# Optimization experiments

Measured on AMD Instinct MI355X. Metric: run time of the kernel, lower is better.

The kernel has to match this reference:

```python
import jax, jax.numpy as jnp
import numpy as np

N_HEAD = 16
N_KV = 4
ROT = 128  # rotary_dim == head_dim
BASE = 10000
N_CTX = 1024


def make_sincos(n_ctx, rotary_dim, base):
    # GPT-NeoX style (rotary_adjacent_pairs=False): freq repeated twice
    pos = jnp.arange(n_ctx, dtype=jnp.float32)
    dim = jnp.arange(rotary_dim // 2, dtype=jnp.float32)
    freq = jnp.float32(base) ** (dim / (rotary_dim / 2))
    freq = jnp.tile(freq, 2)  # [rotary_dim]
    angles = pos[:, None] / freq[None, :]  # [n_ctx, rotary_dim]
    return jnp.sin(angles), jnp.cos(angles)


def setup_inputs() -> dict:
    key = jax.random.key(0)
    ks = jax.random.split(key, 5)
    B, T, C = 8, 1024, 2048
    r = N_HEAD // N_KV
    Ckv = C // r
    s = 0.02
    x = jax.random.normal(ks[0], (B, T, C), jnp.float32)
    wq = jax.random.normal(ks[1], (C, C), jnp.float32) * s
    wk = jax.random.normal(ks[2], (C, Ckv), jnp.float32) * s
    wv = jax.random.normal(ks[3], (C, Ckv), jnp.float32) * s
    wo = jax.random.normal(ks[4], (C, C), jnp.float32) * s
    sin, cos = make_sincos(N_CTX, ROT, BASE)
    return dict(x=x, wq=wq, wk=wk, wv=wv, wo=wo, sin=sin, cos=cos)


def _rope(x, sin, cos):
    # x: [B, H, T, hd]; rotary applied to first ROT dims (here ROT == hd)
    T = x.shape[2]
    n = ROT // 2
    x_rot = x[..., :ROT]
    x_pass = x[..., ROT:]
    # rotate_every_two (NeoX style): [x0..x_{n-1}, x_n..] -> [-x_n.., x0..]
    x_flip = jnp.concatenate([-x_rot[..., n:], x_rot[..., :n]], axis=-1)
    c = cos[None, None, :T, :]
    s = sin[None, None, :T, :]
    x_rotated = x_rot * c + x_flip * s
    return jnp.concatenate([x_rotated, x_pass], axis=-1)


def reference(x, wq, wk, wv, wo, sin, cos):
    B, T, C = x.shape
    H = N_HEAD
    hd = C // H
    r = H // N_KV
    q = (x @ wq).reshape(B, T, H, hd).transpose(0, 2, 1, 3)  # [B,H,T,hd]
    # Original: repeat_interleave along seq dim then view(B,T,H,hd).
    # Equivalent to tiling the kv channel vector r times per position.
    k = jnp.tile(x @ wk, (1, 1, r)).reshape(B, T, H, hd).transpose(0, 2, 1, 3)
    v = jnp.tile(x @ wv, (1, 1, r)).reshape(B, T, H, hd).transpose(0, 2, 1, 3)
    q = _rope(q, sin, cos)
    k = _rope(k, sin, cos)
    att = jnp.einsum('bhqd,bhkd->bhqk', q, k) / jnp.sqrt(jnp.float32(hd))
    causal = jnp.tril(jnp.ones((T, T), dtype=bool))
    att = jnp.where(causal[None, None], att, -jnp.inf)
    att = jax.nn.softmax(att, axis=-1)
    y = jnp.einsum('bhqk,bhkd->bhqd', att, v)
    y = y.transpose(0, 2, 1, 3).reshape(B, T, C)
    return y @ wo
```

## Files before the change

kernel.cpp:

```cpp
#include <hip/hip_runtime.h>

typedef __attribute__((ext_vector_type(8))) short short8;
typedef __attribute__((ext_vector_type(4))) float f32x4;

#define B_    8
#define T_    1024
#define C_    2048
#define H_    16
#define HKV_  4
#define HD_   128
#define M_    8192
#define NQKV_ 3072
#define KDIM_ 2048

__device__ __forceinline__ unsigned short f2bf(float f) {
  unsigned u = __float_as_uint(f);
  u += 0x7FFF + ((u >> 16) & 1);
  return (unsigned short)(u >> 16);
}
__device__ __forceinline__ float bf2f(unsigned short h) {
  return __uint_as_float(((unsigned)h) << 16);
}

__device__ __forceinline__ void async16(const unsigned short* g, unsigned short* l) {
  __builtin_amdgcn_global_load_lds(
      (const unsigned int __attribute__((address_space(1)))*)g,
      (unsigned int __attribute__((address_space(3)))*)l,
      16, 0, 0);
}

__global__ __launch_bounds__(256) void cvt_bf16_kernel(const float* __restrict__ in,
                                                       unsigned short* __restrict__ out) {
  int idx = blockIdx.x * 256 + threadIdx.x;
  float4 v = ((const float4*)in)[idx];
  ushort4 o;
  o.x = f2bf(v.x); o.y = f2bf(v.y); o.z = f2bf(v.z); o.w = f2bf(v.w);
  ((ushort4*)out)[idx] = o;
}

__global__ __launch_bounds__(256) void tpose_f32_bf16(const float* __restrict__ in,
                                                      unsigned short* __restrict__ out,
                                                      int Cc, int ldo) {
  __shared__ unsigned short tile[32][33];
  int c0 = blockIdx.x * 32, r0 = blockIdx.y * 32;
  int tx = threadIdx.x, ty = threadIdx.y;
#pragma unroll
  for (int j = 0; j < 4; j++)
    tile[ty + j * 8][tx] = f2bf(in[(size_t)(r0 + ty + j * 8) * Cc + c0 + tx]);
  __syncthreads();
#pragma unroll
  for (int j = 0; j < 4; j++)
    out[(size_t)(c0 + ty + j * 8) * ldo + r0 + tx] = tile[tx][ty + j * 8];
}

__global__ __launch_bounds__(256) void vtpose(const unsigned short* __restrict__ qkv,
                                              unsigned short* __restrict__ vt) {
  __shared__ unsigned short tile[32][33];
  int b = blockIdx.z;
  int c0 = blockIdx.x * 32, t0 = blockIdx.y * 32;
  int tx = threadIdx.x, ty = threadIdx.y;
  const unsigned short* src = qkv + (size_t)b * T_ * NQKV_ + 2560;
#pragma unroll
  for (int j = 0; j < 4; j++)
    tile[ty + j * 8][tx] = src[(size_t)(t0 + ty + j * 8) * NQKV_ + c0 + tx];
  __syncthreads();
  unsigned short* dst = vt + (size_t)b * 512 * T_;
#pragma unroll
  for (int j = 0; j < 4; j++)
    dst[(size_t)(c0 + ty + j * 8) * T_ + t0 + tx] = tile[tx][ty + j * 8];
}

__global__ __launch_bounds__(256) void rope_kernel(const unsigned short* __restrict__ qkv,
                                                   const float* __restrict__ sinp,
                                                   const float* __restrict__ cosp,
                                                   unsigned short* __restrict__ qatt,
                                                   unsigned short* __restrict__ katt) {
  int m = blockIdx.x;
  int b = m >> 10, t = m & 1023;
  int tid = threadIdx.x;
  int d = tid & 63;
  const unsigned short* row = qkv + (size_t)m * NQKV_;
  float c0 = cosp[t * 128 + d], s0 = sinp[t * 128 + d];
  float c1 = cosp[t * 128 + d + 64], s1 = sinp[t * 128 + d + 64];
#pragma unroll
  for (int h0 = 0; h0 < 16; h0 += 4) {
    int h = h0 + (tid >> 6);
    float x0 = bf2f(row[h * 128 + d]);
    float x1 = bf2f(row[h * 128 + d + 64]);
    size_t o = ((size_t)(b * 16 + h) * 1024 + t) * 128 + d;
    qatt[o]      = f2bf(x0 * c0 - x1 * s0);
    qatt[o + 64] = f2bf(x1 * c1 + x0 * s1);
  }
  {
    int kh = tid >> 6;
    float x0 = bf2f(row[2048 + kh * 128 + d]);
    float x1 = bf2f(row[2048 + kh * 128 + d + 64]);
    size_t o = ((size_t)(b * 4 + kh) * 1024 + t) * 128 + d;
    katt[o]      = f2bf(x0 * c0 - x1 * s0);
    katt[o + 64] = f2bf(x1 * c1 + x0 * s1);
  }
}

template <int OUTF32>
__global__ __launch_bounds__(256) void gemm_bf16(const unsigned short* __restrict__ A,
                                                 const unsigned short* __restrict__ BT,
                                                 void* __restrict__ Cout, int N) {
  __shared__ unsigned short lA[128 * 32];
  __shared__ unsigned short lB[128 * 32];
  const int K = KDIM_;
  int tid = threadIdx.x;
  int lane = tid & 63;
  int w = tid >> 6;
  int quad = lane >> 4, l16 = lane & 15;
  int bm = blockIdx.y, bn = blockIdx.x;
  const unsigned short* Ab = A + (size_t)bm * 128 * K;
  const unsigned short* Bb = BT + (size_t)bn * 128 * K;
  int i0 = tid, i1 = tid + 256;
  int ra0 = i0 >> 2, ca0 = (i0 & 3) * 8;
  int ra1 = i1 >> 2, ca1 = (i1 & 3) * 8;
  int wm = (w >> 1) * 64, wn = (w & 1) * 64;
  f32x4 acc[4][4] = {};
  for (int k0 = 0; k0 < K; k0 += 32) {
    __syncthreads();
    async16(Ab + (size_t)ra0 * K + k0 + ca0, &lA[i0 * 8]);
    async16(Ab + (size_t)ra1 * K + k0 + ca1, &lA[i1 * 8]);
    async16(Bb + (size_t)ra0 * K + k0 + ca0, &lB[i0 * 8]);
    async16(Bb + (size_t)ra1 * K + k0 + ca1, &lB[i1 * 8]);
    __syncthreads();
    short8 af[4], bfr[4];
#pragma unroll
    for (int mt = 0; mt < 4; mt++)
      af[mt] = *(const short8*)&lA[(wm + mt * 16 + l16) * 32 + quad * 8];
#pragma unroll
    for (int nt = 0; nt < 4; nt++)
      bfr[nt] = *(const short8*)&lB[(wn + nt * 16 + l16) * 32 + quad * 8];
#pragma unroll
    for (int mt = 0; mt < 4; mt++)
#pragma unroll
      for (int nt = 0; nt < 4; nt++)
        acc[mt][nt] = __builtin_amdgcn_mfma_f32_16x16x32_bf16(af[mt], bfr[nt], acc[mt][nt], 0, 0, 0);
  }
#pragma unroll
  for (int mt = 0; mt < 4; mt++) {
#pragma unroll
    for (int nt = 0; nt < 4; nt++) {
      int n = bn * 128 + wn + nt * 16 + l16;
#pragma unroll
      for (int r = 0; r < 4; r++) {
        int m = bm * 128 + wm + mt * 16 + quad * 4 + r;
        if (OUTF32)
          ((float*)Cout)[(size_t)m * N + n] = acc[mt][nt][r];
        else
          ((unsigned short*)Cout)[(size_t)m * N + n] = f2bf(acc[mt][nt][r]);
      }
    }
  }
}

__global__ __launch_bounds__(256, 2) void attn_kernel(const unsigned short* __restrict__ Q,
                                                      const unsigned short* __restrict__ Km,
                                                      const unsigned short* __restrict__ Vt,
                                                      unsigned short* __restrict__ Y) {
  __shared__ __align__(16) unsigned short lK[8192];
  __shared__ __align__(16) unsigned short lV[8192];
  int tid = threadIdx.x;
  int lane = tid & 63, w = tid >> 6;
  int quad = lane >> 4, l16 = lane & 15;
  int qt = 7 - blockIdx.x;
  int bh = blockIdx.y;
  int b = bh >> 4, h = bh & 15, kh = h & 3;
  int qrow0 = qt * 128 + w * 32;
  const unsigned short* Qb = Q + ((size_t)bh * T_ + qrow0) * 128;
  const unsigned short* Kb = Km + (size_t)(b * 4 + kh) * T_ * 128;
  const unsigned short* Vb = Vt + (size_t)(b * 4 + kh) * 128 * T_;
  short8 qf[2][4];
#pragma unroll
  for (int mt = 0; mt < 2; mt++)
#pragma unroll
    for (int ks = 0; ks < 4; ks++)
      qf[mt][ks] = *(const short8*)&Qb[(mt * 16 + l16) * 128 + ks * 32 + quad * 8];
  f32x4 o[2][8] = {};
  float m_r[2][4], l_r[2][4];
#pragma unroll
  for (int mt = 0; mt < 2; mt++)
#pragma unroll
    for (int r = 0; r < 4; r++) {
      m_r[mt][r] = -1e30f;
      l_r[mt][r] = 0.f;
    }
  const float sc = 0.12751744690989f;
  unsigned short* pb = &lK[w * 1152];
  const int sw = (l16 & 3) * 8;
  int ntile = 2 * qt + 2;
  for (int kt = 0; kt < ntile; kt++) {
    int n0 = kt * 64;
    __syncthreads();
#pragma unroll
    for (int j = 0; j < 4; j++) {
      int i = tid + j * 256;
      int tq = (i & 3) ^ ((i >> 2) & 3);
      async16(Kb + (size_t)(n0 + ((i >> 2) & 63)) * 128 + (i >> 8) * 32 + tq * 8,
              &lK[i * 8]);
    }
#pragma unroll
    for (int j = 0; j < 4; j++) {
      int i = tid + j * 256;
      int tq = (i & 3) ^ ((i >> 2) & 3);
      async16(Vb + (size_t)((i >> 2) & 127) * T_ + n0 + (i >> 9) * 32 + tq * 8,
              &lV[i * 8]);
    }
    __syncthreads();
    f32x4 s[2][4] = {};
#pragma unroll
    for (int ct = 0; ct < 4; ct++) {
      short8 kf[4];
#pragma unroll
      for (int ks = 0; ks < 4; ks++)
        kf[ks] = *(const short8*)&lK[ks * 2048 + (ct * 16 + l16) * 32 + (quad * 8 ^ sw)];
#pragma unroll
      for (int ks = 0; ks < 4; ks++) {
        s[0][ct] = __builtin_amdgcn_mfma_f32_16x16x32_bf16(qf[0][ks], kf[ks], s[0][ct], 0, 0, 0);
        s[1][ct] = __builtin_amdgcn_mfma_f32_16x16x32_bf16(qf[1][ks], kf[ks], s[1][ct], 0, 0, 0);
      }
    }
#pragma unroll
    for (int mt = 0; mt < 2; mt++)
#pragma unroll
      for (int ct = 0; ct < 4; ct++)
#pragma unroll
        for (int r = 0; r < 4; r++)
          s[mt][ct][r] *= sc;
    if (kt >= 2 * qt) {
#pragma unroll
      for (int mt = 0; mt < 2; mt++)
#pragma unroll
        for (int ct = 0; ct < 4; ct++) {
          int n = n0 + ct * 16 + l16;
#pragma unroll
          for (int r = 0; r < 4; r++) {
            int q = qrow0 + mt * 16 + quad * 4 + r;
            if (n > q) s[mt][ct][r] = -1e30f;
          }
        }
    }
    float alpha[2][4];
#pragma unroll
    for (int mt = 0; mt < 2; mt++)
#pragma unroll
      for (int r = 0; r < 4; r++) {
        float v = fmaxf(fmaxf(s[mt][0][r], s[mt][1][r]), fmaxf(s[mt][2][r], s[mt][3][r]));
#pragma unroll
        for (int off = 1; off < 16; off <<= 1)
          v = fmaxf(v, __shfl_xor(v, off));
        float mn = fmaxf(m_r[mt][r], v);
        alpha[mt][r] = exp2f(m_r[mt][r] - mn);
        m_r[mt][r] = mn;
      }
#pragma unroll
    for (int mt = 0; mt < 2; mt++)
#pragma unroll
      for (int ct = 0; ct < 4; ct++)
#pragma unroll
        for (int r = 0; r < 4; r++)
          s[mt][ct][r] = exp2f(s[mt][ct][r] - m_r[mt][r]);
#pragma unroll
    for (int mt = 0; mt < 2; mt++)
#pragma unroll
      for (int r = 0; r < 4; r++) {
        float v = s[mt][0][r] + s[mt][1][r] + s[mt][2][r] + s[mt][3][r];
#pragma unroll
        for (int off = 1; off < 16; off <<= 1)
          v += __shfl_xor(v, off);
        l_r[mt][r] = l_r[mt][r] * alpha[mt][r] + v;
      }
#pragma unroll
    for (int mt = 0; mt < 2; mt++)
#pragma unroll
      for (int dt = 0; dt < 8; dt++)
#pragma unroll
        for (int r = 0; r < 4; r++)
          o[mt][dt][r] *= alpha[mt][r];
    __syncthreads();
#pragma unroll
    for (int ct = 0; ct < 4; ct++)
#pragma unroll
      for (int r = 0; r < 4; r++)
        pb[(quad * 4 + r) * 72 + ct * 16 + l16] = f2bf(s[0][ct][r]);
    __builtin_amdgcn_s_waitcnt(0xC07F);
    short8 pa0[2];
#pragma unroll
    for (int ks2 = 0; ks2 < 2; ks2++)
      pa0[ks2] = *(const short8*)&pb[l16 * 72 + ks2 * 32 + quad * 8];
    __builtin_amdgcn_s_waitcnt(0xC07F);
    asm volatile("" ::: "memory");
#pragma unroll
    for (int ct = 0; ct < 4; ct++)
#pragma unroll
      for (int r = 0; r < 4; r++)
        pb[(quad * 4 + r) * 72 + ct * 16 + l16] = f2bf(s[1][ct][r]);
    __builtin_amdgcn_s_waitcnt(0xC07F);
    short8 pa1[2];
#pragma unroll
    for (int ks2 = 0; ks2 < 2; ks2++)
      pa1[ks2] = *(const short8*)&pb[l16 * 72 + ks2 * 32 + quad * 8];
#pragma unroll
    for (int dt = 0; dt < 8; dt++) {
#pragma unroll
      for (int ks2 = 0; ks2 < 2; ks2++) {
        short8 vf = *(const short8*)&lV[ks2 * 4096 + (dt * 16 + l16) * 32 + (quad * 8 ^ sw)];
        o[0][dt] = __builtin_amdgcn_mfma_f32_16x16x32_bf16(pa0[ks2], vf, o[0][dt], 0, 0, 0);
        o[1][dt] = __builtin_amdgcn_mfma_f32_16x16x32_bf16(pa1[ks2], vf, o[1][dt], 0, 0, 0);
      }
    }
  }
#pragma unroll
  for (int mt = 0; mt < 2; mt++)
#pragma unroll
    for (int r = 0; r < 4; r++) {
      int q = qrow0 + mt * 16 + quad * 4 + r;
      float inv = 1.f / l_r[mt][r];
      size_t base = ((size_t)(b * 1024 + q)) * 2048 + h * 128 + l16;
#pragma unroll
      for (int dt = 0; dt < 8; dt++)
        Y[base + dt * 16] = f2bf(o[mt][dt][r] * inv);
    }
}

extern "C" void kernel_launch(void* const* d_in, const int* in_sizes, int n_in,
                              void* d_out, int out_size, void* d_ws, size_t ws_size,
                              hipStream_t stream) {
  const float* x    = (const float*)d_in[0];
  const float* wq   = (const float*)d_in[1];
  const float* wk   = (const float*)d_in[2];
  const float* wv   = (const float*)d_in[3];
  const float* wo   = (const float*)d_in[4];
  const float* sinp = (const float*)d_in[5];
  const float* cosp = (const float*)d_in[6];

  char* ws = (char*)d_ws;
  unsigned short* WCATT = (unsigned short*)(ws);
  unsigned short* WOT   = (unsigned short*)(ws + 12582912);
  unsigned short* XBF   = (unsigned short*)(ws + 20971520);
  unsigned short* QKV   = (unsigned short*)(ws + 54525952);
  unsigned short* KATT  = (unsigned short*)(ws + 104857600);
  unsigned short* VT    = (unsigned short*)(ws + 113246208);
  unsigned short* QATT  = XBF;
  unsigned short* Y     = QKV;

  dim3 tb(32, 8);
  cvt_bf16_kernel<<<16384, 256, 0, stream>>>(x, XBF);
  tpose_f32_bf16<<<dim3(64, 64), tb, 0, stream>>>(wq, WCATT, 2048, 2048);
  tpose_f32_bf16<<<dim3(16, 64), tb, 0, stream>>>(wk, WCATT + (size_t)2048 * 2048, 512, 2048);
  tpose_f32_bf16<<<dim3(16, 64), tb, 0, stream>>>(wv, WCATT + (size_t)2560 * 2048, 512, 2048);
  tpose_f32_bf16<<<dim3(64, 64), tb, 0, stream>>>(wo, WOT, 2048, 2048);
  gemm_bf16<0><<<dim3(24, 64), 256, 0, stream>>>(XBF, WCATT, QKV, 3072);
  rope_kernel<<<8192, 256, 0, stream>>>(QKV, sinp, cosp, QATT, KATT);
  vtpose<<<dim3(16, 32, 8), tb, 0, stream>>>(QKV, VT);
  attn_kernel<<<dim3(8, 128), 256, 0, stream>>>(QATT, KATT, VT, Y);
  gemm_bf16<1><<<dim3(16, 64), 256, 0, stream>>>(Y, WOT, d_out, 2048);
}
```

Baseline: 546.2 us.

## Double-buffer K/V tiles in attention and defer row-sum reduction

Attention kernel now double-buffers K and V tiles in LDS: the next tile is prefetched asynchronously while the current one is computed, and there is one barrier per iteration instead of two. The softmax scale is folded into the exp2 argument via fma, and the per-tile row-sum shuffle reduction is deferred to a single reduction after the loop. P staging gets its own LDS buffer, and s_setprio is raised around the MFMA blocks. LDS use grows from 32KB to about 73KB, which may cut occupancy below the two blocks per CU that the launch bounds target.

```diff
diff --git a/kernel.cpp b/kernel.cpp
--- a/kernel.cpp
+++ b/kernel.cpp
@@ -161,8 +161,9 @@
                                                       const unsigned short* __restrict__ Km,
                                                       const unsigned short* __restrict__ Vt,
                                                       unsigned short* __restrict__ Y) {
-  __shared__ __align__(16) unsigned short lK[8192];
-  __shared__ __align__(16) unsigned short lV[8192];
+  __shared__ __align__(16) unsigned short lK[2][8192];
+  __shared__ __align__(16) unsigned short lV[2][8192];
+  __shared__ __align__(16) unsigned short lP[4608];
   int tid = threadIdx.x;
   int lane = tid & 63, w = tid >> 6;
   int quad = lane >> 4, l16 = lane & 15;
@@ -189,47 +190,59 @@
       l_r[mt][r] = 0.f;
     }
   const float sc = 0.12751744690989f;
-  unsigned short* pb = &lK[w * 1152];
+  unsigned short* pb = &lP[w * 1152];
   const int sw = (l16 & 3) * 8;
   int ntile = 2 * qt + 2;
+
+  int krow[4], kcol[4], vrow[4], vcol[4];
+#pragma unroll
+  for (int j = 0; j < 4; j++) {
+    int i = tid + j * 256;
+    int tq = (i & 3) ^ ((i >> 2) & 3);
+    krow[j] = (i >> 2) & 63;
+    kcol[j] = (i >> 8) * 32 + tq * 8;
+    vrow[j] = (i >> 2) & 127;
+    vcol[j] = (i >> 9) * 32 + tq * 8;
+  }
+
+#pragma unroll
+  for (int j = 0; j < 4; j++)
+    async16(Kb + (size_t)krow[j] * 128 + kcol[j], &lK[0][(tid + j * 256) * 8]);
+#pragma unroll
+  for (int j = 0; j < 4; j++)
+    async16(Vb + (size_t)vrow[j] * T_ + vcol[j], &lV[0][(tid + j * 256) * 8]);
+  asm volatile("s_waitcnt vmcnt(0)" ::: "memory");
+  __syncthreads();
+
+  int cur = 0;
   for (int kt = 0; kt < ntile; kt++) {
     int n0 = kt * 64;
-    __syncthreads();
-#pragma unroll
-    for (int j = 0; j < 4; j++) {
-      int i = tid + j * 256;
-      int tq = (i & 3) ^ ((i >> 2) & 3);
-      async16(Kb + (size_t)(n0 + ((i >> 2) & 63)) * 128 + (i >> 8) * 32 + tq * 8,
-              &lK[i * 8]);
-    }
-#pragma unroll
-    for (int j = 0; j < 4; j++) {
-      int i = tid + j * 256;
-      int tq = (i & 3) ^ ((i >> 2) & 3);
-      async16(Vb + (size_t)((i >> 2) & 127) * T_ + n0 + (i >> 9) * 32 + tq * 8,
-              &lV[i * 8]);
-    }
-    __syncthreads();
+    if (kt + 1 < ntile) {
+      int n1 = n0 + 64;
+#pragma unroll
+      for (int j = 0; j < 4; j++)
+        async16(Kb + (size_t)(n1 + krow[j]) * 128 + kcol[j], &lK[cur ^ 1][(tid + j * 256) * 8]);
+#pragma unroll
+      for (int j = 0; j < 4; j++)
+        async16(Vb + (size_t)vrow[j] * T_ + n1 + vcol[j], &lV[cur ^ 1][(tid + j * 256) * 8]);
+    }
+    const unsigned short* lKc = lK[cur];
+    const unsigned short* lVc = lV[cur];
     f32x4 s[2][4] = {};
+    __builtin_amdgcn_s_setprio(1);
 #pragma unroll
     for (int ct = 0; ct < 4; ct++) {
       short8 kf[4];
 #pragma unroll
       for (int ks = 0; ks < 4; ks++)
-        kf[ks] = *(const short8*)&lK[ks * 2048 + (ct * 16 + l16) * 32 + (quad * 8 ^ sw)];
+        kf[ks] = *(const short8*)&lKc[ks * 2048 + (ct * 16 + l16) * 32 + (quad * 8 ^ sw)];
 #pragma unroll
       for (int ks = 0; ks < 4; ks++) {
         s[0][ct] = __builtin_amdgcn_mfma_f32_16x16x32_bf16(qf[0][ks], kf[ks], s[0][ct], 0, 0, 0);
         s[1][ct] = __builtin_amdgcn_mfma_f32_16x16x32_bf16(qf[1][ks], kf[ks], s[1][ct], 0, 0, 0);
       }
     }
-#pragma unroll
-    for (int mt = 0; mt < 2; mt++)
-#pragma unroll
-      for (int ct = 0; ct < 4; ct++)
-#pragma unroll
-        for (int r = 0; r < 4; r++)
-          s[mt][ct][r] *= sc;
+    __builtin_amdgcn_s_setprio(0);
     if (kt >= 2 * qt) {
 #pragma unroll
       for (int mt = 0; mt < 2; mt++)
@@ -243,7 +256,7 @@
           }
         }
     }
-    float alpha[2][4];
+    float alpha[2][4], msc[2][4];
 #pragma unroll
     for (int mt = 0; mt < 2; mt++)
 #pragma unroll
@@ -253,8 +266,9 @@
         for (int off = 1; off < 16; off <<= 1)
           v = fmaxf(v, __shfl_xor(v, off));
         float mn = fmaxf(m_r[mt][r], v);
-        alpha[mt][r] = exp2f(m_r[mt][r] - mn);
+        alpha[mt][r] = exp2f((m_r[mt][r] - mn) * sc);
         m_r[mt][r] = mn;
+        msc[mt][r] = mn * sc;
       }
 #pragma unroll
     for (int mt = 0; mt < 2; mt++)
@@ -262,17 +276,13 @@
       for (int ct = 0; ct < 4; ct++)
 #pragma unroll
         for (int r = 0; r < 4; r++)
-          s[mt][ct][r] = exp2f(s[mt][ct][r] - m_r[mt][r]);
+          s[mt][ct][r] = exp2f(fmaf(s[mt][ct][r], sc, -msc[mt][r]));
 #pragma unroll
     for (int mt = 0; mt < 2; mt++)
 #pragma unroll
-      for (int r = 0; r < 4; r++) {
-        float v = s[mt][0][r] + s[mt][1][r] + s[mt][2][r] + s[mt][3][r];
-#pragma unroll
-        for (int off = 1; off < 16; off <<= 1)
-          v += __shfl_xor(v, off);
-        l_r[mt][r] = l_r[mt][r] * alpha[mt][r] + v;
-      }
+      for (int r = 0; r < 4; r++)
+        l_r[mt][r] = l_r[mt][r] * alpha[mt][r] +
+                     (s[mt][0][r] + s[mt][1][r]) + (s[mt][2][r] + s[mt][3][r]);
 #pragma unroll
     for (int mt = 0; mt < 2; mt++)
 #pragma unroll
@@ -280,7 +290,6 @@
 #pragma unroll
         for (int r = 0; r < 4; r++)
           o[mt][dt][r] *= alpha[mt][r];
-    __syncthreads();
 #pragma unroll
     for (int ct = 0; ct < 4; ct++)
 #pragma unroll
@@ -303,16 +312,33 @@
 #pragma unroll
     for (int ks2 = 0; ks2 < 2; ks2++)
       pa1[ks2] = *(const short8*)&pb[l16 * 72 + ks2 * 32 + quad * 8];
+    __builtin_amdgcn_s_setprio(1);
 #pragma unroll
     for (int dt = 0; dt < 8; dt++) {
 #pragma unroll
       for (int ks2 = 0; ks2 < 2; ks2++) {
-        short8 vf = *(const short8*)&lV[ks2 * 4096 + (dt * 16 + l16) * 32 + (quad * 8 ^ sw)];
+        short8 vf = *(const short8*)&lVc[ks2 * 4096 + (dt * 16 + l16) * 32 + (quad * 8 ^ sw)];
         o[0][dt] = __builtin_amdgcn_mfma_f32_16x16x32_bf16(pa0[ks2], vf, o[0][dt], 0, 0, 0);
         o[1][dt] = __builtin_amdgcn_mfma_f32_16x16x32_bf16(pa1[ks2], vf, o[1][dt], 0, 0, 0);
       }
     }
-  }
+    __builtin_amdgcn_s_setprio(0);
+    if (kt + 1 < ntile) {
+      asm volatile("s_waitcnt vmcnt(0)" ::: "memory");
+      __syncthreads();
+      cur ^= 1;
+    }
+  }
+#pragma unroll
+  for (int mt = 0; mt < 2; mt++)
+#pragma unroll
+    for (int r = 0; r < 4; r++) {
+      float v = l_r[mt][r];
+#pragma unroll
+      for (int off = 1; off < 16; off <<= 1)
+        v += __shfl_xor(v, off);
+      l_r[mt][r] = v;
+    }
 #pragma unroll
   for (int mt = 0; mt < 2; mt++)
 #pragma unroll
```

After: 527.6 us. 3.4% less time.
